# Performance work log

Hardware: AMD Instinct MI355X
Metric: run time of the kernel (lower is better)

Reference implementation:

```python
import jax, jax.numpy as jnp
import numpy as np

B, S, D, H = 2, 4096, 512, 8
HD = D // H  # head_dim = 64


def setup_inputs() -> dict:
    key = jax.random.key(0)
    ks = jax.random.split(key, 13)
    scale = 1.0 / np.sqrt(D)
    inp = {
        "query": jax.random.normal(ks[0], (B, S, D), dtype=jnp.float32),
        "key": jax.random.normal(ks[1], (B, S, D), dtype=jnp.float32),
        "value": jax.random.normal(ks[2], (B, S, D), dtype=jnp.float32),
        "mask": jax.random.randint(ks[3], (B, S, S), 0, 2, dtype=jnp.int32),
        "Wq": jax.random.normal(ks[4], (D, D), dtype=jnp.float32) * scale,
        "bq": jnp.zeros((D,), dtype=jnp.float32),
        "Wk": jax.random.normal(ks[5], (D, D), dtype=jnp.float32) * scale,
        "bk": jnp.zeros((D,), dtype=jnp.float32),
        "Wv": jax.random.normal(ks[6], (D, D), dtype=jnp.float32) * scale,
        "bv": jnp.zeros((D,), dtype=jnp.float32),
        "Wo": jax.random.normal(ks[7], (D, D), dtype=jnp.float32) * scale,
        "bo": jnp.zeros((D,), dtype=jnp.float32),
    }
    return inp


def reference(query, key, value, mask, Wq, bq, Wk, bk, Wv, bv, Wo, bo):
    # Linear projections (torch Linear: x @ W.T + b), split heads: [B,H,S,HD]
    def split_heads(x):
        return x.reshape(B, S, H, HD).transpose(0, 2, 1, 3)

    q = split_heads(query @ Wq.T + bq)
    k = split_heads(key @ Wk.T + bk)
    v = split_heads(value @ Wv.T + bv)

    # NOTE: original module applies NO 1/sqrt(head_dim) scaling.
    scores = jnp.einsum("bhqd,bhkd->bhqk", q, k)  # [B,H,S,S]
    scores = jnp.where(mask[:, None, :, :] == 0, jnp.float32(-1e9), scores)
    probs = jax.nn.softmax(scores, axis=-1)
    attn = jnp.einsum("bhqk,bhkd->bhqd", probs, v)  # [B,H,S,HD]
    attn = attn.transpose(0, 2, 1, 3).reshape(B, S, D)
    return attn @ Wo.T + bo
```

## Files before the change

### kernel.cpp

```cpp
#include <hip/hip_runtime.h>
#include <hip/hip_bf16.h>
#include <cstddef>
#include <cstdint>


#define S_LEN 4096
#define DMODEL 512
#define NHEAD 8
#define HDIM 64
#define NWORDS (S_LEN / 64)

typedef __bf16 bf16x8 __attribute__((ext_vector_type(8)));
typedef _Float16 f16x8 __attribute__((ext_vector_type(8)));
typedef float f32x4 __attribute__((ext_vector_type(4)));
typedef float f32x16 __attribute__((ext_vector_type(16)));
typedef int i32x2 __attribute__((ext_vector_type(2)));
typedef unsigned int u32x4 __attribute__((ext_vector_type(4)));
typedef unsigned short u16x4 __attribute__((ext_vector_type(4)));
typedef unsigned short u16x8 __attribute__((ext_vector_type(8)));

__device__ __forceinline__ unsigned short f2bf(float x) {
  return __builtin_bit_cast(unsigned short, (__bf16)x);
}
__device__ __forceinline__ float bf2f(unsigned short h) {
  union { unsigned u; float f; } v; v.u = ((unsigned)h) << 16; return v.f;
}
__device__ __forceinline__ float fast_exp2(float x) {
#if __has_builtin(__builtin_amdgcn_exp2f)
  return __builtin_amdgcn_exp2f(x);
#else
  return __expf(x * 0.69314718056f);
#endif
}
__device__ __forceinline__ float max3f(float a, float b, float c) {
  return fmaxf(fmaxf(a, b), c);
}
__device__ __forceinline__ int bit_mask(unsigned hs, int bs) {
#if __has_builtin(__builtin_amdgcn_sbfe)
  return __builtin_amdgcn_sbfe((int)hs, bs, 1);
#else
  return ((int)(hs << (31 - bs))) >> 31;
#endif
}
__device__ __forceinline__ float mask_blend(float x, int msk) {
  const int NEG = __builtin_bit_cast(int, -1.0e9f);
  int xi = __builtin_bit_cast(int, x);
  return __builtin_bit_cast(float, (xi & msk) | (NEG & ~msk));
}
__device__ __forceinline__ void pl_swap(int& a, int& b) {
#if __has_builtin(__builtin_amdgcn_permlane32_swap)
  i32x2 r = __builtin_amdgcn_permlane32_swap(a, b, false, false);
  a = r[0]; b = r[1];
#else
  asm volatile("v_permlane32_swap_b32 %0, %1" : "+v"(a), "+v"(b));
#endif
}
__device__ __forceinline__ float xhalf_max(float x) {
  int a = __builtin_bit_cast(int, x), b = a;
  pl_swap(a, b);
  return fmaxf(__builtin_bit_cast(float, a), __builtin_bit_cast(float, b));
}
__device__ __forceinline__ float xhalf_sum(float x) {
  int a = __builtin_bit_cast(int, x), b = a;
  pl_swap(a, b);
  return __builtin_bit_cast(float, a) + __builtin_bit_cast(float, b);
}
__device__ __forceinline__ int swzi(int row, int col) {
  return row * 64 + ((col & 7) | ((((col >> 3) ^ row) & 7) << 3));
}
__device__ __forceinline__ void gload16(const unsigned short* g, unsigned short* lds) {
  __builtin_amdgcn_global_load_lds(
      (const __attribute__((address_space(1))) unsigned int*)g,
      (__attribute__((address_space(3))) unsigned int*)lds, 16, 0, 0);
}

__global__ __launch_bounds__(256) void prep(
    const float* __restrict__ query, const float* __restrict__ key,
    const float* __restrict__ value,
    const float* __restrict__ w0, const float* __restrict__ w1,
    const float* __restrict__ w2, const float* __restrict__ w3,
    const int* __restrict__ mask,
    unsigned short* __restrict__ qh, unsigned short* __restrict__ ql,
    unsigned short* __restrict__ kh, unsigned short* __restrict__ kl,
    unsigned short* __restrict__ vh, unsigned short* __restrict__ vl,
    unsigned short* __restrict__ wbuf, unsigned long long* __restrict__ bits)
{
  const int task = blockIdx.y;
  const int tid = blockIdx.x * 256 + threadIdx.x;
  const int nthr = gridDim.x * 256;

  if (task < 3) {
    const float* x = (task == 0) ? query : (task == 1) ? key : value;
    unsigned short* h = (task == 0) ? qh : (task == 1) ? kh : vh;
    unsigned short* l = (task == 0) ? ql : (task == 1) ? kl : vl;
    const int n4 = (int)((size_t)2 * S_LEN * DMODEL / 4);
    for (int i = tid; i < n4; i += nthr) {
      float4 f = ((const float4*)x)[i];
      float ff[4] = {f.x, f.y, f.z, f.w};
      u16x4 hh, ll;
      #pragma unroll
      for (int j = 0; j < 4; ++j) {
        unsigned short hb = f2bf(ff[j]);
        hh[j] = hb;
        ll[j] = f2bf(ff[j] - bf2f(hb));
      }
      ((u16x4*)h)[i] = hh;
      ((u16x4*)l)[i] = ll;
    }
  } else if (task == 3) {
    const int per = 65536;
    for (int i = tid; i < 4 * per; i += nthr) {
      int wsel = i >> 16, idx = i & (per - 1);
      const float* src = (wsel == 0) ? w0 : (wsel == 1) ? w1 : (wsel == 2) ? w2 : w3;
      unsigned short* h = wbuf + (size_t)wsel * 2 * 262144;
      unsigned short* l = h + 262144;
      float4 f = ((const float4*)src)[idx];
      float ff[4] = {f.x, f.y, f.z, f.w};
      u16x4 hh, ll;
      #pragma unroll
      for (int j = 0; j < 4; ++j) {
        unsigned short hb = f2bf(ff[j]);
        hh[j] = hb;
        ll[j] = f2bf(ff[j] - bf2f(hb));
      }
      ((u16x4*)h)[idx] = hh;
      ((u16x4*)l)[idx] = ll;
    }
  } else {
    const int nwords = 2 * S_LEN * NWORDS;
    int gw = tid >> 6;
    int lane = threadIdx.x & 63;
    int nw = nthr >> 6;
    for (int w = gw; w < nwords; w += nw) {
      int v = mask[(size_t)w * 64 + lane];
      unsigned long long bm = __ballot(v != 0);
      if (lane == 0) bits[w] = bm;
    }
  }
}

__global__ __launch_bounds__(256) void proj_qkv(
    const unsigned short* __restrict__ qxh, const unsigned short* __restrict__ qxl,
    const unsigned short* __restrict__ kxh, const unsigned short* __restrict__ kxl,
    const unsigned short* __restrict__ vxh, const unsigned short* __restrict__ vxl,
    const unsigned short* __restrict__ wbuf,
    const float* __restrict__ bq, const float* __restrict__ bk, const float* __restrict__ bv,
    unsigned short* __restrict__ qout, unsigned short* __restrict__ kout,
    unsigned short* __restrict__ vout)
{
  const int mode = blockIdx.z;
  const bool tri = (mode < 2);
  const unsigned short* xh = (mode == 0) ? qxh : (mode == 1) ? kxh : vxh;
  const unsigned short* xl = (mode == 0) ? qxl : (mode == 1) ? kxl : vxl;
  const unsigned short* wh = wbuf + (size_t)mode * 2 * 262144;
  const unsigned short* wl = wh + 262144;
  const float* bias = (mode == 0) ? bq : (mode == 1) ? bk : bv;
  unsigned short* out = (mode == 0) ? qout : (mode == 1) ? kout : vout;
  const float oscale = (mode == 0) ? 1.44269504f : 1.0f;

  __shared__ __align__(16) unsigned short SMEM[24576];
  unsigned short* Xh = SMEM;
  unsigned short* Xl = SMEM + 8192;
  unsigned short* Wh = SMEM + 16384;
  unsigned short* Wl = SMEM + 20480;

  const int t = threadIdx.x;
  const int lane = t & 63;
  const int w = t >> 6;
  const int c = lane & 15;
  const int g = lane >> 4;
  const int row0 = blockIdx.x * 128;
  const int col0 = blockIdx.y * 64;

  f32x4 acc[2][4];
  #pragma unroll
  for (int mi = 0; mi < 2; ++mi)
    #pragma unroll
    for (int n = 0; n < 4; ++n) acc[mi][n] = (f32x4){0.f, 0.f, 0.f, 0.f};

  u16x8 pxh[4], pxl[4], pwh[2], pwl[2];
  auto issue = [&](int k0) {
    #pragma unroll
    for (int i = 0; i < 4; ++i) {
      int id = i * 256 + t;
      int r = id >> 3, ch = id & 7;
      size_t off = (size_t)(row0 + r) * DMODEL + k0 + ch * 8;
      pxh[i] = *(const u16x8*)(xh + off);
      if (tri) pxl[i] = *(const u16x8*)(xl + off);
    }
    #pragma unroll
    for (int i = 0; i < 2; ++i) {
      int id = i * 256 + t;
      int r = id >> 3, ch = id & 7;
      size_t off = (size_t)(col0 + r) * DMODEL + k0 + ch * 8;
      pwh[i] = *(const u16x8*)(wh + off);
      if (tri) pwl[i] = *(const u16x8*)(wl + off);
    }
  };
  auto commit = [&]() {
    #pragma unroll
    for (int i = 0; i < 4; ++i) {
      int id = i * 256 + t;
      int r = id >> 3, ch = id & 7;
      int dst = r * 64 + (((ch ^ r) & 7) << 3);
      *(u16x8*)&Xh[dst] = pxh[i];
      if (tri) *(u16x8*)&Xl[dst] = pxl[i];
    }
    #pragma unroll
    for (int i = 0; i < 2; ++i) {
      int id = i * 256 + t;
      int r = id >> 3, ch = id & 7;
      int dst = r * 64 + (((ch ^ r) & 7) << 3);
      *(u16x8*)&Wh[dst] = pwh[i];
      if (tri) *(u16x8*)&Wl[dst] = pwl[i];
    }
  };

  issue(0);
  commit();
  __syncthreads();

  for (int k0 = 0; k0 < DMODEL; k0 += 64) {
    const bool more = (k0 + 64) < DMODEL;
    if (more) issue(k0 + 64);

    #pragma unroll
    for (int kk = 0; kk < 2; ++kk) {
      bf16x8 ah[2], al[2], bh_[4], bl_[4];
      #pragma unroll
      for (int mi = 0; mi < 2; ++mi) {
        int r = w * 32 + mi * 16 + c;
        ah[mi] = __builtin_bit_cast(bf16x8, *(const u16x8*)&Xh[swzi(r, (kk * 4 + g) * 8)]);
        if (tri) al[mi] = __builtin_bit_cast(bf16x8, *(const u16x8*)&Xl[swzi(r, (kk * 4 + g) * 8)]);
      }
      #pragma unroll
      for (int n = 0; n < 4; ++n) {
        int r = n * 16 + c;
        bh_[n] = __builtin_bit_cast(bf16x8, *(const u16x8*)&Wh[swzi(r, (kk * 4 + g) * 8)]);
        if (tri) bl_[n] = __builtin_bit_cast(bf16x8, *(const u16x8*)&Wl[swzi(r, (kk * 4 + g) * 8)]);
      }
      #pragma unroll
      for (int mi = 0; mi < 2; ++mi)
        #pragma unroll
        for (int n = 0; n < 4; ++n) {
          acc[mi][n] = __builtin_amdgcn_mfma_f32_16x16x32_bf16(ah[mi], bh_[n], acc[mi][n], 0, 0, 0);
          if (tri) {
            acc[mi][n] = __builtin_amdgcn_mfma_f32_16x16x32_bf16(al[mi], bh_[n], acc[mi][n], 0, 0, 0);
            acc[mi][n] = __builtin_amdgcn_mfma_f32_16x16x32_bf16(ah[mi], bl_[n], acc[mi][n], 0, 0, 0);
          }
        }
    }
    __syncthreads();
    if (more) {
      commit();
      __syncthreads();
    }
  }

  if (mode < 2) {
    #pragma unroll
    for (int mi = 0; mi < 2; ++mi)
      #pragma unroll
      for (int n = 0; n < 4; ++n)
        #pragma unroll
        for (int j = 0; j < 4; ++j) {
          int rr = row0 + w * 32 + mi * 16 + g * 4 + j;
          int oo = col0 + n * 16 + c;
          float val = (acc[mi][n][j] + bias[oo]) * oscale;
          int bb = rr >> 12, ss = rr & (S_LEN - 1), h2 = oo >> 6, hd = oo & 63;
          size_t idx = (((size_t)(bb * NHEAD + h2)) * S_LEN + ss) * HDIM + hd;
          out[idx] = __builtin_bit_cast(unsigned short, (_Float16)val);
        }
  } else {
    unsigned short* Ts = SMEM;
    __syncthreads();
    #pragma unroll
    for (int mi = 0; mi < 2; ++mi)
      #pragma unroll
      for (int n = 0; n < 4; ++n)
        #pragma unroll
        for (int j = 0; j < 4; ++j) {
          int r = w * 32 + mi * 16 + g * 4 + j;
          int o = n * 16 + c;
          Ts[r * 68 + o] = __builtin_bit_cast(unsigned short, (_Float16)(acc[mi][n][j] + bias[col0 + o]));
        }
    __syncthreads();
    int bb = row0 >> 12, sbase = row0 & (S_LEN - 1), h2 = col0 >> 6;
    int d = t >> 2, s0 = (t & 3) * 32;
    size_t obase = ((size_t)((bb * NHEAD + h2) * HDIM + d)) * S_LEN + sbase + s0;
    #pragma unroll
    for (int i = 0; i < 4; ++i) {
      u16x8 v;
      #pragma unroll
      for (int jj = 0; jj < 8; ++jj) v[jj] = Ts[(s0 + i * 8 + jj) * 68 + d];
      *(u16x8*)(out + obase + i * 8) = v;
    }
  }
}

__global__ __launch_bounds__(256) void gemm_out(
    const unsigned short* __restrict__ xh, const unsigned short* __restrict__ wh,
    const float* __restrict__ bias, float* __restrict__ Y)
{
  __shared__ __align__(16) unsigned short SMEM[24576];
  unsigned short* Xh = SMEM;
  unsigned short* Wh = SMEM + 16384;

  const int t = threadIdx.x;
  const int lane = t & 63;
  const int w = t >> 6;
  const int c = lane & 15;
  const int g = lane >> 4;
  const int row0 = blockIdx.x * 128;
  const int col0 = blockIdx.y * 64;

  f32x4 acc[2][4];
  #pragma unroll
  for (int mi = 0; mi < 2; ++mi)
    #pragma unroll
    for (int n = 0; n < 4; ++n) acc[mi][n] = (f32x4){0.f, 0.f, 0.f, 0.f};

  u16x8 pxh[4], pwh[2];
  auto issue = [&](int k0) {
    #pragma unroll
    for (int i = 0; i < 4; ++i) {
      int id = i * 256 + t;
      int r = id >> 3, ch = id & 7;
      pxh[i] = *(const u16x8*)(xh + (size_t)(row0 + r) * DMODEL + k0 + ch * 8);
    }
    #pragma unroll
    for (int i = 0; i < 2; ++i) {
      int id = i * 256 + t;
      int r = id >> 3, ch = id & 7;
      pwh[i] = *(const u16x8*)(wh + (size_t)(col0 + r) * DMODEL + k0 + ch * 8);
    }
  };
  auto commit = [&]() {
    #pragma unroll
    for (int i = 0; i < 4; ++i) {
      int id = i * 256 + t;
      int r = id >> 3, ch = id & 7;
      *(u16x8*)&Xh[r * 64 + (((ch ^ r) & 7) << 3)] = pxh[i];
    }
    #pragma unroll
    for (int i = 0; i < 2; ++i) {
      int id = i * 256 + t;
      int r = id >> 3, ch = id & 7;
      *(u16x8*)&Wh[r * 64 + (((ch ^ r) & 7) << 3)] = pwh[i];
    }
  };

  issue(0);
  commit();
  __syncthreads();

  for (int k0 = 0; k0 < DMODEL; k0 += 64) {
    const bool more = (k0 + 64) < DMODEL;
    if (more) issue(k0 + 64);

    #pragma unroll
    for (int kk = 0; kk < 2; ++kk) {
      bf16x8 ah[2], bh_[4];
      #pragma unroll
      for (int mi = 0; mi < 2; ++mi)
        ah[mi] = __builtin_bit_cast(bf16x8, *(const u16x8*)&Xh[swzi(w * 32 + mi * 16 + c, (kk * 4 + g) * 8)]);
      #pragma unroll
      for (int n = 0; n < 4; ++n)
        bh_[n] = __builtin_bit_cast(bf16x8, *(const u16x8*)&Wh[swzi(n * 16 + c, (kk * 4 + g) * 8)]);
      #pragma unroll
      for (int mi = 0; mi < 2; ++mi)
        #pragma unroll
        for (int n = 0; n < 4; ++n)
          acc[mi][n] = __builtin_amdgcn_mfma_f32_16x16x32_bf16(ah[mi], bh_[n], acc[mi][n], 0, 0, 0);
    }
    __syncthreads();
    if (more) {
      commit();
      __syncthreads();
    }
  }

  #pragma unroll
  for (int mi = 0; mi < 2; ++mi)
    #pragma unroll
    for (int n = 0; n < 4; ++n)
      #pragma unroll
      for (int j = 0; j < 4; ++j) {
        int rr = row0 + w * 32 + mi * 16 + g * 4 + j;
        int oo = col0 + n * 16 + c;
        Y[(size_t)rr * DMODEL + oo] = acc[mi][n][j] + bias[oo];
      }
}

__global__ __launch_bounds__(256) void attn32(
    const unsigned short* __restrict__ qf, const unsigned short* __restrict__ kf,
    const unsigned short* __restrict__ vt, const unsigned long long* __restrict__ mbits,
    unsigned short* __restrict__ Ob)
{
  __shared__ __align__(16) unsigned short LDS[2][2][4096];

  const int t = threadIdx.x;
  const int lane = t & 63;
  const int w = t >> 6;
  const int pair = w >> 1;
  const int chunk = w & 1;
  const int c31 = lane & 31;
  const int hi = lane >> 5;

  const int nwg = gridDim.x;
  const int bid = blockIdx.x;
  const int lin = (bid & 7) * (nwg >> 3) + (bid >> 3);
  const int qi = lin & 63;
  const int bh = lin >> 6;
  const int q0 = qi * 64;
  const int b = bh >> 3, h = bh & 7;
  const int qrow = q0 + pair * 32 + c31;

  const unsigned short* Qp = qf + ((size_t)bh * S_LEN + qrow) * HDIM;
  f16x8 qfr[4];
  #pragma unroll
  for (int s = 0; s < 4; ++s)
    qfr[s] = __builtin_bit_cast(f16x8, *(const u16x8*)(Qp + 16 * s + 8 * hi));

  const unsigned short* Kb = kf + (size_t)bh * S_LEN * HDIM;
  const unsigned short* Vbt = vt + (size_t)bh * HDIM * S_LEN;
  const unsigned long long* mptr = mbits + (size_t)(b * S_LEN + qrow) * NWORDS;

  const int idx0 = (w * 2 + 0) * 64 + lane;
  const int idx1 = (w * 2 + 1) * 64 + lane;
  const int r0 = idx0 >> 3, r1 = idx1 >> 3;
  const int c0 = ((lane & 7) ^ r0) & 7, c1 = ((lane & 7) ^ r1) & 7;
  const unsigned short* nK0 = Kb + r0 * HDIM + c0 * 8;
  const unsigned short* nK1 = Kb + r1 * HDIM + c1 * 8;
  const unsigned short* nV0 = Vbt + (size_t)r0 * S_LEN + c0 * 8;
  const unsigned short* nV1 = Vbt + (size_t)r1 * S_LEN + c1 * 8;
  const int ld0 = (w * 2 + 0) * 512;
  const int ld1 = (w * 2 + 1) * 512;

  auto issue = [&](int buf) {
    gload16(nK0, &LDS[buf][0][ld0]);
    gload16(nK1, &LDS[buf][0][ld1]);
    gload16(nV0, &LDS[buf][1][ld0]);
    gload16(nV1, &LDS[buf][1][ld1]);
    nK0 += 64 * HDIM; nK1 += 64 * HDIM;
    nV0 += 64; nV1 += 64;
  };

  f32x16 oacc0, oacc1;
  #pragma unroll
  for (int r = 0; r < 16; ++r) { oacc0[r] = 0.f; oacc1[r] = 0.f; }
  const f32x16 fzero = oacc0;
  float mrow = -INFINITY, lrow = 0.f;

  unsigned long long m64 = mptr[0], m64n = 0;

  issue(0);
  __syncthreads();

  int cur = 0;
  for (int kt = 0; kt < S_LEN / 64; ++kt) {
    const bool more = kt < (S_LEN / 64 - 1);
    if (more) {
      issue(cur ^ 1);
      m64n = mptr[kt + 1];
    }
    const unsigned short* K_ = &LDS[cur][0][0];
    const unsigned short* Vt_ = &LDS[cur][1][0];

    f32x16 p;
    __builtin_amdgcn_s_setprio(1);
    {
      int idx = swzi(chunk * 32 + c31, 8 * hi);
      f16x8 kfr = __builtin_bit_cast(f16x8, *(const u16x8*)&K_[idx]);
      p = __builtin_amdgcn_mfma_f32_32x32x16_f16(kfr, qfr[0], fzero, 0, 0, 0);
    }
    #pragma unroll
    for (int s = 1; s < 4; ++s) {
      int idx = swzi(chunk * 32 + c31, 16 * s + 8 * hi);
      f16x8 kfr = __builtin_bit_cast(f16x8, *(const u16x8*)&K_[idx]);
      p = __builtin_amdgcn_mfma_f32_32x32x16_f16(kfr, qfr[s], p, 0, 0, 0);
    }
    __builtin_amdgcn_s_setprio(0);

    unsigned half = chunk ? (unsigned)(m64 >> 32) : (unsigned)m64;
    unsigned hs = half >> (hi * 4);
    #pragma unroll
    for (int r = 0; r < 16; ++r) {
      int bs = (r & 3) + 8 * (r >> 2);
      p[r] = mask_blend(p[r], bit_mask(hs, bs));
    }

    float t0 = max3f(p[0], p[1], p[2]);
    float t1 = max3f(p[3], p[4], p[5]);
    float t2 = max3f(p[6], p[7], p[8]);
    float t3 = max3f(p[9], p[10], p[11]);
    float t4 = max3f(p[12], p[13], p[14]);
    float mx = fmaxf(max3f(t0, t1, t2), max3f(t3, t4, p[15]));
    mx = xhalf_max(mx);

    float mn, scl;
    if (__all(mx <= mrow + 11.54f)) {
      mn = mrow;
      scl = 1.0f;
    } else {
      mn = fmaxf(mrow, mx);
      scl = fast_exp2(mrow - mn);
      mrow = mn;
      oacc0 *= scl;
      oacc1 *= scl;
    }

    #pragma unroll
    for (int r = 0; r < 16; ++r) p[r] = fast_exp2(p[r] - mn);

    float s0_ = (p[0] + p[1]) + (p[2] + p[3]);
    float s1_ = (p[4] + p[5]) + (p[6] + p[7]);
    float s2_ = (p[8] + p[9]) + (p[10] + p[11]);
    float s3_ = (p[12] + p[13]) + (p[14] + p[15]);
    float ps = xhalf_sum((s0_ + s1_) + (s2_ + s3_));
    lrow = lrow * scl + ps;

    unsigned W[4][2];
    #pragma unroll
    for (int rq = 0; rq < 4; ++rq) {
      W[rq][0] = __builtin_bit_cast(unsigned, __builtin_amdgcn_cvt_pkrtz(p[4 * rq + 0], p[4 * rq + 1]));
      W[rq][1] = __builtin_bit_cast(unsigned, __builtin_amdgcn_cvt_pkrtz(p[4 * rq + 2], p[4 * rq + 3]));
    }
    f16x8 pf[2];
    #pragma unroll
    for (int s2 = 0; s2 < 2; ++s2) {
      unsigned keep0 = hi ? W[2 * s2 + 1][0] : W[2 * s2][0];
      unsigned keep1 = hi ? W[2 * s2 + 1][1] : W[2 * s2][1];
      unsigned send0 = hi ? W[2 * s2][0] : W[2 * s2 + 1][0];
      unsigned send1 = hi ? W[2 * s2][1] : W[2 * s2 + 1][1];
      unsigned recv0 = (unsigned)__shfl_xor((int)send0, 32, 64);
      unsigned recv1 = (unsigned)__shfl_xor((int)send1, 32, 64);
      u32x4 fw;
      fw[0] = hi ? recv0 : keep0;
      fw[1] = hi ? recv1 : keep1;
      fw[2] = hi ? keep0 : recv0;
      fw[3] = hi ? keep1 : recv1;
      pf[s2] = __builtin_bit_cast(f16x8, fw);
    }

    __builtin_amdgcn_s_setprio(1);
    #pragma unroll
    for (int s2 = 0; s2 < 2; ++s2) {
      int col = chunk * 32 + 16 * s2 + 8 * hi;
      f16x8 vf0 = __builtin_bit_cast(f16x8, *(const u16x8*)&Vt_[swzi(c31, col)]);
      f16x8 vf1 = __builtin_bit_cast(f16x8, *(const u16x8*)&Vt_[swzi(32 + c31, col)]);
      oacc0 = __builtin_amdgcn_mfma_f32_32x32x16_f16(vf0, pf[s2], oacc0, 0, 0, 0);
      oacc1 = __builtin_amdgcn_mfma_f32_32x32x16_f16(vf1, pf[s2], oacc1, 0, 0, 0);
    }
    __builtin_amdgcn_s_setprio(0);

    if (more) m64 = m64n;
    __syncthreads();
    cur ^= 1;
  }

  float* mb = (float*)&LDS[0][0][0];
  const int mi = ((pair * 2 + hi) * 32 + c31) * 36;
  if (chunk == 1) {
    #pragma unroll
    for (int q4 = 0; q4 < 4; ++q4) {
      *(f32x4*)&mb[mi + q4 * 4]      = (f32x4){oacc0[q4 * 4], oacc0[q4 * 4 + 1], oacc0[q4 * 4 + 2], oacc0[q4 * 4 + 3]};
      *(f32x4*)&mb[mi + 16 + q4 * 4] = (f32x4){oacc1[q4 * 4], oacc1[q4 * 4 + 1], oacc1[q4 * 4 + 2], oacc1[q4 * 4 + 3]};
    }
    mb[mi + 32] = mrow;
    mb[mi + 33] = lrow;
  }
  __syncthreads();
  if (chunk == 0) {
    float m1 = mb[mi + 32], l1 = mb[mi + 33];
    float mS = fmaxf(mrow, m1);
    float f0 = fast_exp2(mrow - mS), f1 = fast_exp2(m1 - mS);
    float lS = lrow * f0 + l1 * f1;
    float inv = 1.0f / lS;
    size_t obase = ((size_t)b * S_LEN + qrow) * DMODEL + h * HDIM;
    #pragma unroll
    for (int c2 = 0; c2 < 2; ++c2) {
      #pragma unroll
      for (int rq = 0; rq < 4; ++rq) {
        u16x4 hv;
        #pragma unroll
        for (int rb = 0; rb < 4; ++rb) {
          int reg = 4 * rq + rb;
          float o0 = (c2 == 0) ? oacc0[reg] : oacc1[reg];
          float o1 = mb[mi + c2 * 16 + reg];
          hv[rb] = f2bf((o0 * f0 + o1 * f1) * inv);
        }
        *(u16x4*)(Ob + obase + 32 * c2 + 8 * rq + 4 * hi) = hv;
      }
    }
  }
}

extern "C" void kernel_launch(void* const* d_in, const int* in_sizes, int n_in,
                              void* d_out, int out_size, void* d_ws, size_t ws_size,
                              hipStream_t stream) {
  const float* query = (const float*)d_in[0];
  const float* key   = (const float*)d_in[1];
  const float* value = (const float*)d_in[2];
  const int*   mask  = (const int*)  d_in[3];
  const float* Wq = (const float*)d_in[4];
  const float* bq = (const float*)d_in[5];
  const float* Wk = (const float*)d_in[6];
  const float* bk = (const float*)d_in[7];
  const float* Wv = (const float*)d_in[8];
  const float* bv = (const float*)d_in[9];
  const float* Wo = (const float*)d_in[10];
  const float* bo = (const float*)d_in[11];
  float* out = (float*)d_out;

  const size_t PER = (size_t)2 * S_LEN * DMODEL;
  const size_t WSZ = (size_t)DMODEL * DMODEL;

  unsigned short* p = (unsigned short*)d_ws;
  unsigned short* wbuf = p;
  unsigned short* xh = p + 8 * WSZ;
  unsigned short* xl = xh + PER;
  unsigned short* yh = xl + PER;
  unsigned short* yl = yh + PER;
  unsigned short* zh = yl + PER;
  unsigned short* zl = zh + PER;
  unsigned short* qfb = zl + PER;
  unsigned short* kfb = qfb + PER;
  unsigned short* vtb = kfb + PER;

  unsigned short* woh = wbuf + 3 * 2 * WSZ;

  unsigned long long* bits = (unsigned long long*)d_out;

  prep<<<dim3(2048, 5), 256, 0, stream>>>(query, key, value, Wq, Wk, Wv, Wo, mask,
                                          xh, xl, yh, yl, zh, zl, wbuf, bits);

  proj_qkv<<<dim3(2 * S_LEN / 128, DMODEL / 64, 3), 256, 0, stream>>>(
      xh, xl, yh, yl, zh, zl, wbuf, bq, bk, bv, qfb, kfb, vtb);

  attn32<<<1024, 256, 0, stream>>>(qfb, kfb, vtb, bits, xh);

  gemm_out<<<dim3(2 * S_LEN / 128, DMODEL / 64), 256, 0, stream>>>(xh, woh, bo, out);
}
```

Measured before the change: 245.7 us.

## Split attention key range into two halves and merge partial results

The attention kernel now launches twice as many blocks, each processing half of the key/value sequence. Each block writes unnormalized fp32 partial outputs plus running max and sum to scratch buffers. A new merge kernel then rescales and combines the two halves and writes the bf16 attention output. The aim is more parallelism and better tail balancing across CUs, at the cost of an extra kernel launch, extra fp32 scratch traffic, and a second pass over the Q fragments.

```diff
diff --git a/kernel.cpp b/kernel.cpp
--- a/kernel.cpp
+++ b/kernel.cpp
@@ -9,6 +9,8 @@
 #define NHEAD 8
 #define HDIM 64
 #define NWORDS (S_LEN / 64)
+#define SHALF 2048
+#define NTILE (SHALF / 64)
 
 typedef __bf16 bf16x8 __attribute__((ext_vector_type(8)));
 typedef _Float16 f16x8 __attribute__((ext_vector_type(8)));
@@ -395,7 +397,7 @@
 __global__ __launch_bounds__(256) void attn32(
     const unsigned short* __restrict__ qf, const unsigned short* __restrict__ kf,
     const unsigned short* __restrict__ vt, const unsigned long long* __restrict__ mbits,
-    unsigned short* __restrict__ Ob)
+    float* __restrict__ part, float* __restrict__ mlb)
 {
   __shared__ __align__(16) unsigned short LDS[2][2][4096];
 
@@ -411,10 +413,12 @@
   const int bid = blockIdx.x;
   const int lin = (bid & 7) * (nwg >> 3) + (bid >> 3);
   const int qi = lin & 63;
-  const int bh = lin >> 6;
+  const int bh = (lin >> 6) & 15;
+  const int half = lin >> 10;
   const int q0 = qi * 64;
   const int b = bh >> 3, h = bh & 7;
   const int qrow = q0 + pair * 32 + c31;
+  const size_t PERF32 = (size_t)2 * S_LEN * DMODEL;
 
   const unsigned short* Qp = qf + ((size_t)bh * S_LEN + qrow) * HDIM;
   f16x8 qfr[4];
@@ -424,16 +428,17 @@
 
   const unsigned short* Kb = kf + (size_t)bh * S_LEN * HDIM;
   const unsigned short* Vbt = vt + (size_t)bh * HDIM * S_LEN;
-  const unsigned long long* mptr = mbits + (size_t)(b * S_LEN + qrow) * NWORDS;
+  const unsigned long long* mptr =
+      mbits + (size_t)(b * S_LEN + qrow) * NWORDS + half * NTILE;
 
   const int idx0 = (w * 2 + 0) * 64 + lane;
   const int idx1 = (w * 2 + 1) * 64 + lane;
   const int r0 = idx0 >> 3, r1 = idx1 >> 3;
   const int c0 = ((lane & 7) ^ r0) & 7, c1 = ((lane & 7) ^ r1) & 7;
-  const unsigned short* nK0 = Kb + r0 * HDIM + c0 * 8;
-  const unsigned short* nK1 = Kb + r1 * HDIM + c1 * 8;
-  const unsigned short* nV0 = Vbt + (size_t)r0 * S_LEN + c0 * 8;
-  const unsigned short* nV1 = Vbt + (size_t)r1 * S_LEN + c1 * 8;
+  const unsigned short* nK0 = Kb + (size_t)(half * SHALF + r0) * HDIM + c0 * 8;
+  const unsigned short* nK1 = Kb + (size_t)(half * SHALF + r1) * HDIM + c1 * 8;
+  const unsigned short* nV0 = Vbt + (size_t)r0 * S_LEN + half * SHALF + c0 * 8;
+  const unsigned short* nV1 = Vbt + (size_t)r1 * S_LEN + half * SHALF + c1 * 8;
   const int ld0 = (w * 2 + 0) * 512;
   const int ld1 = (w * 2 + 1) * 512;
 
@@ -458,8 +463,8 @@
   __syncthreads();
 
   int cur = 0;
-  for (int kt = 0; kt < S_LEN / 64; ++kt) {
-    const bool more = kt < (S_LEN / 64 - 1);
+  for (int kt = 0; kt < NTILE; ++kt) {
+    const bool more = kt < (NTILE - 1);
     if (more) {
       issue(cur ^ 1);
       m64n = mptr[kt + 1];
@@ -482,8 +487,8 @@
     }
     __builtin_amdgcn_s_setprio(0);
 
-    unsigned half = chunk ? (unsigned)(m64 >> 32) : (unsigned)m64;
-    unsigned hs = half >> (hi * 4);
+    unsigned halfw = chunk ? (unsigned)(m64 >> 32) : (unsigned)m64;
+    unsigned hs = halfw >> (hi * 4);
     #pragma unroll
     for (int r = 0; r < 16; ++r) {
       int bs = (r & 3) + 8 * (r >> 2);
@@ -576,24 +581,56 @@
     float mS = fmaxf(mrow, m1);
     float f0 = fast_exp2(mrow - mS), f1 = fast_exp2(m1 - mS);
     float lS = lrow * f0 + l1 * f1;
-    float inv = 1.0f / lS;
-    size_t obase = ((size_t)b * S_LEN + qrow) * DMODEL + h * HDIM;
+    float* po = part + (size_t)half * PERF32 + ((size_t)b * S_LEN + qrow) * DMODEL + h * HDIM;
     #pragma unroll
     for (int c2 = 0; c2 < 2; ++c2) {
       #pragma unroll
       for (int rq = 0; rq < 4; ++rq) {
-        u16x4 hv;
+        f32x4 v;
         #pragma unroll
         for (int rb = 0; rb < 4; ++rb) {
           int reg = 4 * rq + rb;
           float o0 = (c2 == 0) ? oacc0[reg] : oacc1[reg];
           float o1 = mb[mi + c2 * 16 + reg];
-          hv[rb] = f2bf((o0 * f0 + o1 * f1) * inv);
+          v[rb] = o0 * f0 + o1 * f1;
         }
-        *(u16x4*)(Ob + obase + 32 * c2 + 8 * rq + 4 * hi) = hv;
+        *(f32x4*)(po + 32 * c2 + 8 * rq + 4 * hi) = v;
       }
     }
+    if (hi == 0) {
+      size_t mli = (((size_t)half * 16 + bh) * S_LEN + qrow) * 2;
+      mlb[mli] = mS;
+      mlb[mli + 1] = lS;
+    }
   }
+}
+
+__global__ __launch_bounds__(256) void merge_halves(
+    const float* __restrict__ part, const float* __restrict__ mlb,
+    unsigned short* __restrict__ Ob)
+{
+  const size_t PERF32 = (size_t)2 * S_LEN * DMODEL;
+  int idx4 = blockIdx.x * 256 + threadIdx.x;
+  int row = idx4 >> 7;
+  int col4 = idx4 & 127;
+  int h = col4 >> 4;
+  int b = row >> 12;
+  int s = row & (S_LEN - 1);
+  int bh = b * NHEAD + h;
+
+  size_t mli = ((size_t)bh * S_LEN + s) * 2;
+  float m0 = mlb[mli], l0 = mlb[mli + 1];
+  float m1 = mlb[(size_t)16 * S_LEN * 2 + mli], l1 = mlb[(size_t)16 * S_LEN * 2 + mli + 1];
+  float mf = fmaxf(m0, m1);
+  float f0 = fast_exp2(m0 - mf), f1 = fast_exp2(m1 - mf);
+  float inv = 1.0f / (l0 * f0 + l1 * f1);
+
+  f32x4 p0 = *(const f32x4*)(part + (size_t)idx4 * 4);
+  f32x4 p1 = *(const f32x4*)(part + PERF32 + (size_t)idx4 * 4);
+  u16x4 o;
+  #pragma unroll
+  for (int j = 0; j < 4; ++j) o[j] = f2bf((p0[j] * f0 + p1[j] * f1) * inv);
+  *(u16x4*)(Ob + (size_t)idx4 * 4) = o;
 }
 
 extern "C" void kernel_launch(void* const* d_in, const int* in_sizes, int n_in,
@@ -638,7 +675,12 @@
   proj_qkv<<<dim3(2 * S_LEN / 128, DMODEL / 64, 3), 256, 0, stream>>>(
       xh, xl, yh, yl, zh, zl, wbuf, bq, bk, bv, qfb, kfb, vtb);
 
-  attn32<<<1024, 256, 0, stream>>>(qfb, kfb, vtb, bits, xh);
+  float* part = (float*)xl;
+  float* mlb  = (float*)zl;
+
+  attn32<<<2048, 256, 0, stream>>>(qfb, kfb, vtb, bits, part, mlb);
+
+  merge_halves<<<(int)(PER / 4 / 256), 256, 0, stream>>>(part, mlb, xh);
 
   gemm_out<<<dim3(2 * S_LEN / 128, DMODEL / 64), 256, 0, stream>>>(xh, woh, bo, out);
 }
```

After: 251.4 us. 1.02x slower.
